# Kernel tuning notes

Measured on AMD Instinct MI355X. Metric: run time of the kernel, lower is better.

## Reference

```python
import jax, jax.numpy as jnp
import numpy as np

N_ENT = 50000
N_REL2 = 100   # num_relations * 2
N_BASES = 16
DIM = 64
N_EDGES = 100000


def _rgcn_conv(x, edge_index, edge_type, edge_norm, basis, att, root, bias):
    # x: [N, D]; basis: [B, D, D]; att: [R, B]; root: [D, D]; bias: [D]
    src = edge_index[0]
    dst = edge_index[1]
    num_nodes = x.shape[0]
    # Per-edge relation weight is w[edge_type] with w = att @ basis (reshaped).
    # By linearity we contract x_j with each basis first, then mix with the
    # per-edge attention coefficients -- same math, avoids the [E, D, D] gather.
    coeff = att[edge_type]                          # [E, B]
    xb = jnp.einsum('ei,bio->ebo', x[src], basis)   # [E, B, D]
    msg = jnp.einsum('eb,ebo->eo', coeff, xb)       # [E, D]
    msg = msg * edge_norm[:, None]
    # scatter-mean aggregation at target nodes
    s = jax.ops.segment_sum(msg, dst, num_segments=num_nodes)
    cnt = jax.ops.segment_sum(jnp.ones((msg.shape[0],), msg.dtype), dst,
                              num_segments=num_nodes)
    agg = s / jnp.maximum(cnt, 1.0)[:, None]
    # root transform + bias
    return agg + x @ root + bias


def setup_inputs() -> dict:
    key = jax.random.key(0)
    ks = jax.random.split(key, 12)
    E = N_EDGES
    inp = {
        'entity': jnp.arange(N_ENT, dtype=jnp.int64) if jax.config.jax_enable_x64 else jnp.arange(N_ENT, dtype=jnp.int32),
        'edge_index': jax.random.randint(ks[0], (2, E), 0, N_ENT),
        'edge_type': jax.random.randint(ks[1], (E,), 0, N_REL2),
        'edge_norm': jax.random.uniform(ks[2], (E,), dtype=jnp.float32),
        'emb': jax.random.normal(ks[3], (N_ENT, DIM), dtype=jnp.float32) * 0.1,
        'basis1': jax.random.normal(ks[4], (N_BASES, DIM, DIM), dtype=jnp.float32) * 0.05,
        'att1': jax.random.normal(ks[5], (N_REL2, N_BASES), dtype=jnp.float32) * 0.1,
        'root1': jax.random.normal(ks[6], (DIM, DIM), dtype=jnp.float32) * 0.05,
        'bias1': jnp.zeros((DIM,), dtype=jnp.float32),
        'basis2': jax.random.normal(ks[7], (N_BASES, DIM, DIM), dtype=jnp.float32) * 0.05,
        'att2': jax.random.normal(ks[8], (N_REL2, N_BASES), dtype=jnp.float32) * 0.1,
        'root2': jax.random.normal(ks[9], (DIM, DIM), dtype=jnp.float32) * 0.05,
        'bias2': jnp.zeros((DIM,), dtype=jnp.float32),
    }
    return inp


def reference(entity, edge_index, edge_type, edge_norm, emb,
              basis1, att1, root1, bias1, basis2, att2, root2, bias2):
    x = emb[entity]                                  # embedding lookup [N, D]
    x = _rgcn_conv(x, edge_index, edge_type, edge_norm, basis1, att1, root1, bias1)
    x = _rgcn_conv(x, edge_index, edge_type, edge_norm, basis2, att2, root2, bias2)
    return x
```

## Files before the change

kernel.cpp:

```cpp
#include <hip/hip_runtime.h>

#define NN 50000
#define NR 100
#define NB 16
#define D  64
#define NE 100000

#define HB  196
#define EPB 512

#define CHUNK 128
#define GROUPS 2
#define EGRID 1024

#define NPB 128
#define NGRID ((NN + NPB - 1) / NPB)

typedef float f32x4  __attribute__((ext_vector_type(4)));
typedef short bf16x8 __attribute__((ext_vector_type(8)));

__device__ __forceinline__ short f2bf(float f) {
    unsigned u = __float_as_uint(f);
    return (short)((u + 0x7FFFu + ((u >> 16) & 1u)) >> 16);
}

__device__ __forceinline__ bf16x8 pack8(f32x4 a, f32x4 b) {
    bf16x8 t;
    t[0] = f2bf(a.x); t[1] = f2bf(a.y); t[2] = f2bf(a.z); t[3] = f2bf(a.w);
    t[4] = f2bf(b.x); t[5] = f2bf(b.y); t[6] = f2bf(b.z); t[7] = f2bf(b.w);
    return t;
}

__global__ __launch_bounds__(256) void compute_wt(
    const float* __restrict__ att1, const float* __restrict__ basis1,
    const float* __restrict__ root1,
    const float* __restrict__ att2, const float* __restrict__ basis2,
    const float* __restrict__ root2,
    float* __restrict__ Wt1, float* __restrict__ Wt2,
    float* __restrict__ rT1, float* __restrict__ rT2)
{
    __shared__ float t[64 * 65];
    int b = blockIdx.x;
    if (b < 2 * NR) {
        int layer = b >= NR;
        int r = layer ? b - NR : b;
        const float* att   = layer ? att2 : att1;
        const float* basis = layer ? basis2 : basis1;
        float*       Wt    = layer ? Wt2 : Wt1;
        float a[NB];
#pragma unroll
        for (int bb = 0; bb < NB; ++bb) a[bb] = att[r * NB + bb];
#pragma unroll
        for (int i = 0; i < 16; ++i) {
            int idx = i * 256 + threadIdx.x;
            float acc = 0.f;
#pragma unroll
            for (int bb = 0; bb < NB; ++bb) acc += a[bb] * basis[bb * 4096 + idx];
            t[(idx >> 6) * 65 + (idx & 63)] = acc;
        }
        __syncthreads();
#pragma unroll
        for (int i = 0; i < 16; ++i) {
            int j = i * 256 + threadIdx.x;
            Wt[(size_t)r * 4096 + j] = t[(j & 63) * 65 + (j >> 6)];
        }
    } else {
        const float* root = (b == 2 * NR) ? root1 : root2;
        float*       rT   = (b == 2 * NR) ? rT1 : rT2;
#pragma unroll
        for (int i = 0; i < 16; ++i) {
            int idx = i * 256 + threadIdx.x;
            t[(idx >> 6) * 65 + (idx & 63)] = root[idx];
        }
        __syncthreads();
#pragma unroll
        for (int i = 0; i < 16; ++i) {
            int j = i * 256 + threadIdx.x;
            rT[j] = t[(j & 63) * 65 + (j >> 6)];
        }
    }
}

__global__ __launch_bounds__(256) void gather_zero(
    const int* __restrict__ entity, const f32x4* __restrict__ emb4,
    f32x4* __restrict__ x04, f32x4* __restrict__ s4, f32x4* __restrict__ cnt4)
{
    int idx = blockIdx.x * 256 + threadIdx.x;
    if (idx >= NN * 16) return;
    int n = idx >> 4;
    int q = idx & 15;
    f32x4 z = {0.f, 0.f, 0.f, 0.f};
    x04[idx] = emb4[(size_t)entity[n] * 16 + q];
    s4[idx] = z;
    if (idx < NN / 4) cnt4[idx] = z;
}

__global__ __launch_bounds__(256) void hist_edges(
    const int* __restrict__ et, const int* __restrict__ dst,
    int* __restrict__ blockHist, float* __restrict__ cnt)
{
    __shared__ int lh[NR];
    for (int i = threadIdx.x; i < NR; i += 256) lh[i] = 0;
    __syncthreads();
#pragma unroll
    for (int i = 0; i < EPB / 256; ++i) {
        int e = blockIdx.x * EPB + i * 256 + threadIdx.x;
        if (e < NE) {
            atomicAdd(&lh[et[e]], 1);
            atomicAdd(&cnt[dst[e]], 1.0f);
        }
    }
    __syncthreads();
    for (int i = threadIdx.x; i < NR; i += 256)
        blockHist[blockIdx.x * NR + i] = lh[i];
}

__global__ __launch_bounds__(256) void colscan(
    const int* __restrict__ blockHist, int* __restrict__ blockPrefix,
    int* __restrict__ relTot)
{
    __shared__ int sc[256];
    int r = blockIdx.x;
    int t = threadIdx.x;
    int v = (t < HB) ? blockHist[t * NR + r] : 0;
    sc[t] = v;
    __syncthreads();
#pragma unroll
    for (int off = 1; off < 256; off <<= 1) {
        int a = (t >= off) ? sc[t - off] : 0;
        __syncthreads();
        sc[t] += a;
        __syncthreads();
    }
    if (t < HB) blockPrefix[t * NR + r] = sc[t] - v;
    if (t == 0) relTot[r] = sc[255];
}

__global__ __launch_bounds__(256) void scanK(
    const int* __restrict__ relTot, int* __restrict__ offs,
    int* __restrict__ nbG, int* __restrict__ tabR, int* __restrict__ tabS)
{
    __shared__ int totL[NR];
    __shared__ int offL[NR + 1];
    __shared__ int cnbL[NR + 1];
    int t = threadIdx.x;
    if (t < NR) totL[t] = relTot[t];
    __syncthreads();
    if (t == 0) {
        int off = 0, cb = 0;
        for (int r = 0; r < NR; ++r) {
            offL[r] = off; cnbL[r] = cb;
            off += totL[r];
            cb  += (totL[r] + CHUNK - 1) / CHUNK;
        }
        offL[NR] = off; cnbL[NR] = cb;
    }
    __syncthreads();
    if (t <= NR) offs[t] = offL[t];
    if (t == 0) nbG[0] = cnbL[NR];
    int nb = cnbL[NR];
    for (int e = t; e < nb; e += 256) {
        int lo = 0, hi = NR;
        while (hi - lo > 1) { int mid = (lo + hi) >> 1; if (cnbL[mid] <= e) lo = mid; else hi = mid; }
        tabR[e] = lo;
        tabS[e] = offL[lo] + (e - cnbL[lo]) * CHUNK;
    }
}

__global__ __launch_bounds__(256) void scatter_sorted(
    const int* __restrict__ src, const int* __restrict__ dst,
    const int* __restrict__ et, const float* __restrict__ en,
    const int* __restrict__ offs, const int* __restrict__ blockPrefix,
    int* __restrict__ srcS, int* __restrict__ dstS, float* __restrict__ normS)
{
    __shared__ int lcur[NR];
    for (int i = threadIdx.x; i < NR; i += 256)
        lcur[i] = offs[i] + blockPrefix[blockIdx.x * NR + i];
    __syncthreads();
#pragma unroll
    for (int i = 0; i < EPB / 256; ++i) {
        int e = blockIdx.x * EPB + i * 256 + threadIdx.x;
        if (e < NE) {
            int r = et[e];
            int p = atomicAdd(&lcur[r], 1);
            srcS[p] = src[e]; dstS[p] = dst[e]; normS[p] = en[e];
        }
    }
}

__global__ __launch_bounds__(256, 4) void edge_mfma(
    const int* __restrict__ srcS, const int* __restrict__ dstS,
    const float* __restrict__ normS, const int* __restrict__ offs,
    const int* __restrict__ tabR, const int* __restrict__ tabS,
    const int* __restrict__ nbG, const float* __restrict__ x,
    const float* __restrict__ Wt, float* __restrict__ s)
{
    __shared__ float LW[64 * 68];
    int b = blockIdx.x;
    if (b >= nbG[0]) return;
    int r  = tabR[b];
    int cs = tabS[b];
    int tid = threadIdx.x;

    {
        const f32x4* __restrict__ Wg = (const f32x4*)(Wt + (size_t)r * 4096);
#pragma unroll
        for (int i = 0; i < 4; ++i) {
            int v = tid + i * 256;
            int d = v >> 4, k4 = v & 15;
            *(f32x4*)(LW + d * 68 + k4 * 4) = Wg[v];
        }
    }
    __syncthreads();

    int lane = tid & 63, wid = tid >> 6;
    int c15 = lane & 15, kg = lane >> 4;

    bf16x8 B[4][2];
#pragma unroll
    for (int nt = 0; nt < 4; ++nt)
#pragma unroll
        for (int ks = 0; ks < 2; ++ks) {
            const f32x4* p = (const f32x4*)(LW + (nt * 16 + c15) * 68 + ks * 32 + kg * 8);
            B[nt][ks] = pack8(p[0], p[1]);
        }

    int segE = offs[r + 1];
    int bend = cs + CHUNK < segE ? cs + CHUNK : segE;

#pragma unroll 1
    for (int g = 0; g < GROUPS; ++g) {
        int gs = cs + wid * (GROUPS * 16) + g * 16;
        if (gs >= bend) break;
        int ge = gs + 16 < bend ? gs + 16 : bend;

        int e  = gs + c15;
        int ec = e < ge ? e : ge - 1;
        float nrm = (e < ge) ? normS[ec] : 0.f;
        int   sn  = srcS[ec];

        const f32x4* xr  = (const f32x4*)(x + (size_t)sn * 64 + kg * 8);
        const f32x4* xr2 = (const f32x4*)(x + (size_t)sn * 64 + 32 + kg * 8);
        bf16x8 A0 = pack8(xr[0]  * nrm, xr[1]  * nrm);
        bf16x8 A1 = pack8(xr2[0] * nrm, xr2[1] * nrm);

        f32x4 z = {0.f, 0.f, 0.f, 0.f};
        f32x4 acc[4] = {z, z, z, z};
#pragma unroll
        for (int nt = 0; nt < 4; ++nt) {
            acc[nt] = __builtin_amdgcn_mfma_f32_16x16x32_bf16(A0, B[nt][0], acc[nt], 0, 0, 0);
            acc[nt] = __builtin_amdgcn_mfma_f32_16x16x32_bf16(A1, B[nt][1], acc[nt], 0, 0, 0);
        }

        int dn[4];
#pragma unroll
        for (int j = 0; j < 4; ++j) {
            int er = gs + kg * 4 + j;
            dn[j] = (er < ge) ? dstS[er] : -1;
        }
#pragma unroll
        for (int nt = 0; nt < 4; ++nt)
#pragma unroll
            for (int j = 0; j < 4; ++j)
                if (dn[j] >= 0)
                    atomicAdd(&s[(size_t)dn[j] * 64 + nt * 16 + c15], acc[nt][j]);
    }
}

__global__ __launch_bounds__(256, 4) void node_mfma(
    const float* __restrict__ x, float* __restrict__ s,
    const float* __restrict__ cnt, const float* __restrict__ rT,
    const float* __restrict__ bias, float* __restrict__ out, int zero_s)
{
    __shared__ float LW[64 * 68];
    int tid = threadIdx.x;
    {
        const f32x4* __restrict__ Rg = (const f32x4*)rT;
#pragma unroll
        for (int i = 0; i < 4; ++i) {
            int v = tid + i * 256;
            int d = v >> 4, k4 = v & 15;
            *(f32x4*)(LW + d * 68 + k4 * 4) = Rg[v];
        }
    }
    __syncthreads();

    int lane = tid & 63, wid = tid >> 6;
    int c15 = lane & 15, kg = lane >> 4;

    bf16x8 B[4][2];
#pragma unroll
    for (int nt = 0; nt < 4; ++nt)
#pragma unroll
        for (int ks = 0; ks < 2; ++ks) {
            const f32x4* p = (const f32x4*)(LW + (nt * 16 + c15) * 68 + ks * 32 + kg * 8);
            B[nt][ks] = pack8(p[0], p[1]);
        }
    float bv[4];
#pragma unroll
    for (int nt = 0; nt < 4; ++nt) bv[nt] = bias[nt * 16 + c15];

#pragma unroll 1
    for (int g = 0; g < GROUPS; ++g) {
        int gs = blockIdx.x * NPB + wid * (GROUPS * 16) + g * 16;
        if (gs >= NN) break;
        int ge = gs + 16 < NN ? gs + 16 : NN;

        int n  = gs + c15;
        int nc = n < ge ? n : ge - 1;
        const f32x4* xr  = (const f32x4*)(x + (size_t)nc * 64 + kg * 8);
        const f32x4* xr2 = (const f32x4*)(x + (size_t)nc * 64 + 32 + kg * 8);
        bf16x8 A0 = pack8(xr[0], xr[1]);
        bf16x8 A1 = pack8(xr2[0], xr2[1]);

        f32x4 z = {0.f, 0.f, 0.f, 0.f};
        f32x4 acc[4] = {z, z, z, z};
#pragma unroll
        for (int nt = 0; nt < 4; ++nt) {
            acc[nt] = __builtin_amdgcn_mfma_f32_16x16x32_bf16(A0, B[nt][0], acc[nt], 0, 0, 0);
            acc[nt] = __builtin_amdgcn_mfma_f32_16x16x32_bf16(A1, B[nt][1], acc[nt], 0, 0, 0);
        }

        float cv[4];
#pragma unroll
        for (int j = 0; j < 4; ++j) {
            int nr = gs + kg * 4 + j;
            cv[j] = (nr < ge) ? cnt[nr] : 1.f;
        }
#pragma unroll
        for (int nt = 0; nt < 4; ++nt)
#pragma unroll
            for (int j = 0; j < 4; ++j) {
                int nr = gs + kg * 4 + j;
                if (nr < ge) {
                    size_t off = (size_t)nr * 64 + nt * 16 + c15;
                    float c = cv[j] > 1.f ? cv[j] : 1.f;
                    out[off] = s[off] / c + acc[nt][j] + bv[nt];
                    if (zero_s) s[off] = 0.f;
                }
            }
    }
}

extern "C" void kernel_launch(void* const* d_in, const int* in_sizes, int n_in,
                              void* d_out, int out_size, void* d_ws, size_t ws_size,
                              hipStream_t stream) {
    const int*   entity    = (const int*)d_in[0];
    const int*   edge_index= (const int*)d_in[1];
    const int*   edge_type = (const int*)d_in[2];
    const float* edge_norm = (const float*)d_in[3];
    const float* emb       = (const float*)d_in[4];
    const float* basis1    = (const float*)d_in[5];
    const float* att1      = (const float*)d_in[6];
    const float* root1     = (const float*)d_in[7];
    const float* bias1     = (const float*)d_in[8];
    const float* basis2    = (const float*)d_in[9];
    const float* att2      = (const float*)d_in[10];
    const float* root2     = (const float*)d_in[11];
    const float* bias2     = (const float*)d_in[12];

    const int* src = edge_index;
    const int* dst = edge_index + NE;

    float* ws    = (float*)d_ws;
    float* Wt1   = ws;
    float* Wt2   = Wt1 + (size_t)NR * 4096;
    float* rT1   = Wt2 + (size_t)NR * 4096;
    float* rT2   = rT1 + 4096;
    float* x0    = rT2 + 4096;
    float* s     = x0  + (size_t)NN * D;
    float* cnt   = s   + (size_t)NN * D;
    float* normS = cnt + NN;
    int*   offs        = (int*)(normS + NE);
    int*   relTot      = offs + NR + 3;
    int*   nbG         = relTot + NR;
    int*   blockHist   = nbG + 3;
    int*   blockPrefix = blockHist + HB * NR;
    int*   tabR        = blockPrefix + HB * NR;
    int*   tabS        = tabR + EGRID;
    int*   srcS        = tabS + EGRID;
    int*   dstS        = srcS + NE;

    float* out = (float*)d_out;

    compute_wt<<<2 * NR + 2, 256, 0, stream>>>(att1, basis1, root1,
                                               att2, basis2, root2,
                                               Wt1, Wt2, rT1, rT2);
    gather_zero<<<(NN * 16 + 255) / 256, 256, 0, stream>>>(
        entity, (const f32x4*)emb, (f32x4*)x0, (f32x4*)s, (f32x4*)cnt);
    hist_edges<<<HB, 256, 0, stream>>>(edge_type, dst, blockHist, cnt);
    colscan<<<NR, 256, 0, stream>>>(blockHist, blockPrefix, relTot);
    scanK<<<1, 256, 0, stream>>>(relTot, offs, nbG, tabR, tabS);
    scatter_sorted<<<HB, 256, 0, stream>>>(src, dst, edge_type, edge_norm,
                                           offs, blockPrefix, srcS, dstS, normS);

    edge_mfma<<<EGRID, 256, 0, stream>>>(srcS, dstS, normS, offs,
                                         tabR, tabS, nbG, x0, Wt1, s);
    node_mfma<<<NGRID, 256, 0, stream>>>(x0, s, cnt, rT1, bias1, out, 1);

    edge_mfma<<<EGRID, 256, 0, stream>>>(srcS, dstS, normS, offs,
                                         tabR, tabS, nbG, out, Wt2, s);
    node_mfma<<<NGRID, 256, 0, stream>>>(out, s, cnt, rT2, bias2, out, 0);
}
```

Baseline: 127.6 us.

## Replace atomic scatter-add with CSR gather aggregation by destination node

Edge kernels now write per-edge messages to a dense msg buffer instead of doing float atomics into s. A per-destination CSR index (degree histogram, node prefix scan, dstIdx permutation) is built during preprocessing, and node_mfma gathers and averages incoming messages per node before adding the root transform. Zeroing of s and cnt is dropped and the embedding gather is merged into the weight-prep kernel. The aim is to remove atomic contention on the aggregation. In exchange it writes and re-reads a 100000x64 message buffer and uses a serial per-node gather loop with uneven degrees.

```diff
diff --git a/kernel.cpp b/kernel.cpp
--- a/kernel.cpp
+++ b/kernel.cpp
@@ -8,6 +8,8 @@
 
 #define HB  196
 #define EPB 512
+#define ZB  196
+#define GB  ((NN * 16 + 255) / 256)
 
 #define CHUNK 128
 #define GROUPS 2
@@ -31,13 +33,15 @@
     return t;
 }
 
-__global__ __launch_bounds__(256) void compute_wt(
+__global__ __launch_bounds__(256) void prep_all(
     const float* __restrict__ att1, const float* __restrict__ basis1,
     const float* __restrict__ root1,
     const float* __restrict__ att2, const float* __restrict__ basis2,
     const float* __restrict__ root2,
+    const int* __restrict__ entity, const f32x4* __restrict__ emb4,
     float* __restrict__ Wt1, float* __restrict__ Wt2,
-    float* __restrict__ rT1, float* __restrict__ rT2)
+    float* __restrict__ rT1, float* __restrict__ rT2,
+    f32x4* __restrict__ x04, int* __restrict__ deg, int* __restrict__ nodeCur)
 {
     __shared__ float t[64 * 65];
     int b = blockIdx.x;
@@ -64,7 +68,7 @@
             int j = i * 256 + threadIdx.x;
             Wt[(size_t)r * 4096 + j] = t[(j & 63) * 65 + (j >> 6)];
         }
-    } else {
+    } else if (b < 2 * NR + 2) {
         const float* root = (b == 2 * NR) ? root1 : root2;
         float*       rT   = (b == 2 * NR) ? rT1 : rT2;
 #pragma unroll
@@ -78,26 +82,22 @@
             int j = i * 256 + threadIdx.x;
             rT[j] = t[(j & 63) * 65 + (j >> 6)];
         }
-    }
-}
-
-__global__ __launch_bounds__(256) void gather_zero(
-    const int* __restrict__ entity, const f32x4* __restrict__ emb4,
-    f32x4* __restrict__ x04, f32x4* __restrict__ s4, f32x4* __restrict__ cnt4)
-{
-    int idx = blockIdx.x * 256 + threadIdx.x;
-    if (idx >= NN * 16) return;
-    int n = idx >> 4;
-    int q = idx & 15;
-    f32x4 z = {0.f, 0.f, 0.f, 0.f};
-    x04[idx] = emb4[(size_t)entity[n] * 16 + q];
-    s4[idx] = z;
-    if (idx < NN / 4) cnt4[idx] = z;
+    } else if (b < 2 * NR + 2 + ZB) {
+        int i = (b - (2 * NR + 2)) * 256 + threadIdx.x;
+        deg[i] = 0; nodeCur[i] = 0;
+    } else {
+        int idx = (b - (2 * NR + 2 + ZB)) * 256 + threadIdx.x;
+        if (idx < NN * 16) {
+            int n = idx >> 4;
+            int q = idx & 15;
+            x04[idx] = emb4[(size_t)entity[n] * 16 + q];
+        }
+    }
 }
 
 __global__ __launch_bounds__(256) void hist_edges(
     const int* __restrict__ et, const int* __restrict__ dst,
-    int* __restrict__ blockHist, float* __restrict__ cnt)
+    int* __restrict__ blockHist, int* __restrict__ deg)
 {
     __shared__ int lh[NR];
     for (int i = threadIdx.x; i < NR; i += 256) lh[i] = 0;
@@ -107,7 +107,7 @@
         int e = blockIdx.x * EPB + i * 256 + threadIdx.x;
         if (e < NE) {
             atomicAdd(&lh[et[e]], 1);
-            atomicAdd(&cnt[dst[e]], 1.0f);
+            atomicAdd(&deg[dst[e]], 1);
         }
     }
     __syncthreads();
@@ -115,36 +115,59 @@
         blockHist[blockIdx.x * NR + i] = lh[i];
 }
 
-__global__ __launch_bounds__(256) void colscan(
+__global__ __launch_bounds__(256) void scans(
     const int* __restrict__ blockHist, int* __restrict__ blockPrefix,
-    int* __restrict__ relTot)
+    int* __restrict__ relTot, const int* __restrict__ deg,
+    int* __restrict__ nodePre, int* __restrict__ blockSumN)
 {
     __shared__ int sc[256];
-    int r = blockIdx.x;
     int t = threadIdx.x;
-    int v = (t < HB) ? blockHist[t * NR + r] : 0;
-    sc[t] = v;
-    __syncthreads();
-#pragma unroll
-    for (int off = 1; off < 256; off <<= 1) {
-        int a = (t >= off) ? sc[t - off] : 0;
-        __syncthreads();
-        sc[t] += a;
-        __syncthreads();
-    }
-    if (t < HB) blockPrefix[t * NR + r] = sc[t] - v;
-    if (t == 0) relTot[r] = sc[255];
+    if (blockIdx.x < NR) {
+        int r = blockIdx.x;
+        int v = (t < HB) ? blockHist[t * NR + r] : 0;
+        sc[t] = v;
+        __syncthreads();
+#pragma unroll
+        for (int off = 1; off < 256; off <<= 1) {
+            int a = (t >= off) ? sc[t - off] : 0;
+            __syncthreads();
+            sc[t] += a;
+            __syncthreads();
+        }
+        if (t < HB) blockPrefix[t * NR + r] = sc[t] - v;
+        if (t == 0) relTot[r] = sc[255];
+    } else {
+        int b = blockIdx.x - NR;
+        int n = b * 256 + t;
+        int v = deg[n];
+        sc[t] = v;
+        __syncthreads();
+#pragma unroll
+        for (int off = 1; off < 256; off <<= 1) {
+            int a = (t >= off) ? sc[t - off] : 0;
+            __syncthreads();
+            sc[t] += a;
+            __syncthreads();
+        }
+        nodePre[n] = sc[t] - v;
+        if (t == 255) blockSumN[b] = sc[255];
+    }
 }
 
 __global__ __launch_bounds__(256) void scanK(
-    const int* __restrict__ relTot, int* __restrict__ offs,
-    int* __restrict__ nbG, int* __restrict__ tabR, int* __restrict__ tabS)
+    const int* __restrict__ relTot, const int* __restrict__ blockSumN,
+    int* __restrict__ offs, int* __restrict__ nbG,
+    int* __restrict__ tabR, int* __restrict__ tabS,
+    int* __restrict__ nodeBlockBase)
 {
     __shared__ int totL[NR];
     __shared__ int offL[NR + 1];
     __shared__ int cnbL[NR + 1];
+    __shared__ int sc2[256];
     int t = threadIdx.x;
     if (t < NR) totL[t] = relTot[t];
+    int v2 = (t < ZB) ? blockSumN[t] : 0;
+    sc2[t] = v2;
     __syncthreads();
     if (t == 0) {
         int off = 0, cb = 0;
@@ -156,6 +179,15 @@
         offL[NR] = off; cnbL[NR] = cb;
     }
     __syncthreads();
+#pragma unroll
+    for (int off = 1; off < 256; off <<= 1) {
+        int a = (t >= off) ? sc2[t - off] : 0;
+        __syncthreads();
+        sc2[t] += a;
+        __syncthreads();
+    }
+    if (t < ZB) nodeBlockBase[t] = sc2[t] - v2;
+    if (t == 0) nodeBlockBase[ZB] = sc2[255];
     if (t <= NR) offs[t] = offL[t];
     if (t == 0) nbG[0] = cnbL[NR];
     int nb = cnbL[NR];
@@ -167,11 +199,13 @@
     }
 }
 
-__global__ __launch_bounds__(256) void scatter_sorted(
+__global__ __launch_bounds__(256) void scatter2(
     const int* __restrict__ src, const int* __restrict__ dst,
     const int* __restrict__ et, const float* __restrict__ en,
     const int* __restrict__ offs, const int* __restrict__ blockPrefix,
-    int* __restrict__ srcS, int* __restrict__ dstS, float* __restrict__ normS)
+    const int* __restrict__ nodePre, const int* __restrict__ nodeBlockBase,
+    int* __restrict__ nodeCur, int* __restrict__ srcS,
+    float* __restrict__ normS, int* __restrict__ dstIdx)
 {
     __shared__ int lcur[NR];
     for (int i = threadIdx.x; i < NR; i += 256)
@@ -183,17 +217,20 @@
         if (e < NE) {
             int r = et[e];
             int p = atomicAdd(&lcur[r], 1);
-            srcS[p] = src[e]; dstS[p] = dst[e]; normS[p] = en[e];
+            srcS[p] = src[e]; normS[p] = en[e];
+            int n = dst[e];
+            int q = nodeBlockBase[n >> 8] + nodePre[n] + atomicAdd(&nodeCur[n], 1);
+            dstIdx[q] = p;
         }
     }
 }
 
 __global__ __launch_bounds__(256, 4) void edge_mfma(
-    const int* __restrict__ srcS, const int* __restrict__ dstS,
-    const float* __restrict__ normS, const int* __restrict__ offs,
-    const int* __restrict__ tabR, const int* __restrict__ tabS,
-    const int* __restrict__ nbG, const float* __restrict__ x,
-    const float* __restrict__ Wt, float* __restrict__ s)
+    const int* __restrict__ srcS, const float* __restrict__ normS,
+    const int* __restrict__ offs, const int* __restrict__ tabR,
+    const int* __restrict__ tabS, const int* __restrict__ nbG,
+    const float* __restrict__ x, const float* __restrict__ Wt,
+    float* __restrict__ msg)
 {
     __shared__ float LW[64 * 68];
     int b = blockIdx.x;
@@ -251,28 +288,25 @@
             acc[nt] = __builtin_amdgcn_mfma_f32_16x16x32_bf16(A0, B[nt][0], acc[nt], 0, 0, 0);
             acc[nt] = __builtin_amdgcn_mfma_f32_16x16x32_bf16(A1, B[nt][1], acc[nt], 0, 0, 0);
         }
-
-        int dn[4];
-#pragma unroll
-        for (int j = 0; j < 4; ++j) {
-            int er = gs + kg * 4 + j;
-            dn[j] = (er < ge) ? dstS[er] : -1;
-        }
 #pragma unroll
         for (int nt = 0; nt < 4; ++nt)
 #pragma unroll
-            for (int j = 0; j < 4; ++j)
-                if (dn[j] >= 0)
-                    atomicAdd(&s[(size_t)dn[j] * 64 + nt * 16 + c15], acc[nt][j]);
+            for (int j = 0; j < 4; ++j) {
+                int er = gs + kg * 4 + j;
+                if (er < ge)
+                    msg[(size_t)er * 64 + nt * 16 + c15] = acc[nt][j];
+            }
     }
 }
 
 __global__ __launch_bounds__(256, 4) void node_mfma(
-    const float* __restrict__ x, float* __restrict__ s,
-    const float* __restrict__ cnt, const float* __restrict__ rT,
-    const float* __restrict__ bias, float* __restrict__ out, int zero_s)
+    const float* __restrict__ x, const float* __restrict__ msg,
+    const int* __restrict__ dstIdx, const int* __restrict__ nodePre,
+    const int* __restrict__ nodeBlockBase, const float* __restrict__ rT,
+    const float* __restrict__ bias, float* __restrict__ out)
 {
     __shared__ float LW[64 * 68];
+    __shared__ float aggL[4][32][68];
     int tid = threadIdx.x;
     {
         const f32x4* __restrict__ Rg = (const f32x4*)rT;
@@ -300,9 +334,28 @@
 #pragma unroll
     for (int nt = 0; nt < 4; ++nt) bv[nt] = bias[nt * 16 + c15];
 
+    int wbase = blockIdx.x * NPB + wid * 32;
+    if (wbase >= NN) return;
+
 #pragma unroll 1
-    for (int g = 0; g < GROUPS; ++g) {
-        int gs = blockIdx.x * NPB + wid * (GROUPS * 16) + g * 16;
+    for (int ln = 0; ln < 32; ++ln) {
+        int n = wbase + ln;
+        if (n >= NN) break;
+        int blk  = n >> 8;
+        int base = nodeBlockBase[blk];
+        int lo = base + nodePre[n];
+        int hi = ((n & 255) == 255) ? nodeBlockBase[blk + 1] : base + nodePre[n + 1];
+        float acc = 0.f;
+        for (int q = lo; q < hi; ++q)
+            acc += msg[(size_t)dstIdx[q] * 64 + lane];
+        float c = (float)(hi - lo);
+        c = c > 1.f ? c : 1.f;
+        aggL[wid][ln][lane] = acc / c;
+    }
+
+#pragma unroll 1
+    for (int g = 0; g < 2; ++g) {
+        int gs = wbase + g * 16;
         if (gs >= NN) break;
         int ge = gs + 16 < NN ? gs + 16 : NN;
 
@@ -320,24 +373,14 @@
             acc[nt] = __builtin_amdgcn_mfma_f32_16x16x32_bf16(A0, B[nt][0], acc[nt], 0, 0, 0);
             acc[nt] = __builtin_amdgcn_mfma_f32_16x16x32_bf16(A1, B[nt][1], acc[nt], 0, 0, 0);
         }
-
-        float cv[4];
-#pragma unroll
-        for (int j = 0; j < 4; ++j) {
-            int nr = gs + kg * 4 + j;
-            cv[j] = (nr < ge) ? cnt[nr] : 1.f;
-        }
 #pragma unroll
         for (int nt = 0; nt < 4; ++nt)
 #pragma unroll
             for (int j = 0; j < 4; ++j) {
                 int nr = gs + kg * 4 + j;
-                if (nr < ge) {
-                    size_t off = (size_t)nr * 64 + nt * 16 + c15;
-                    float c = cv[j] > 1.f ? cv[j] : 1.f;
-                    out[off] = s[off] / c + acc[nt][j] + bv[nt];
-                    if (zero_s) s[off] = 0.f;
-                }
+                if (nr < ge)
+                    out[(size_t)nr * 64 + nt * 16 + c15] =
+                        aggL[wid][g * 16 + kg * 4 + j][nt * 16 + c15] + acc[nt][j] + bv[nt];
             }
     }
 }
@@ -368,9 +411,8 @@
     float* rT1   = Wt2 + (size_t)NR * 4096;
     float* rT2   = rT1 + 4096;
     float* x0    = rT2 + 4096;
-    float* s     = x0  + (size_t)NN * D;
-    float* cnt   = s   + (size_t)NN * D;
-    float* normS = cnt + NN;
+    float* msg   = x0  + (size_t)NN * D;
+    float* normS = msg + (size_t)NE * D;
     int*   offs        = (int*)(normS + NE);
     int*   relTot      = offs + NR + 3;
     int*   nbG         = relTot + NR;
@@ -379,26 +421,34 @@
     int*   tabR        = blockPrefix + HB * NR;
     int*   tabS        = tabR + EGRID;
     int*   srcS        = tabS + EGRID;
-    int*   dstS        = srcS + NE;
+    int*   deg         = srcS + NE;
+    int*   nodePre     = deg + ZB * 256;
+    int*   nodeCur     = nodePre + ZB * 256;
+    int*   blockSumN   = nodeCur + ZB * 256;
+    int*   nodeBB      = blockSumN + ZB + 4;
+    int*   dstIdx      = nodeBB + ZB + 5;
 
     float* out = (float*)d_out;
 
-    compute_wt<<<2 * NR + 2, 256, 0, stream>>>(att1, basis1, root1,
-                                               att2, basis2, root2,
-                                               Wt1, Wt2, rT1, rT2);
-    gather_zero<<<(NN * 16 + 255) / 256, 256, 0, stream>>>(
-        entity, (const f32x4*)emb, (f32x4*)x0, (f32x4*)s, (f32x4*)cnt);
-    hist_edges<<<HB, 256, 0, stream>>>(edge_type, dst, blockHist, cnt);
-    colscan<<<NR, 256, 0, stream>>>(blockHist, blockPrefix, relTot);
-    scanK<<<1, 256, 0, stream>>>(relTot, offs, nbG, tabR, tabS);
-    scatter_sorted<<<HB, 256, 0, stream>>>(src, dst, edge_type, edge_norm,
-                                           offs, blockPrefix, srcS, dstS, normS);
-
-    edge_mfma<<<EGRID, 256, 0, stream>>>(srcS, dstS, normS, offs,
-                                         tabR, tabS, nbG, x0, Wt1, s);
-    node_mfma<<<NGRID, 256, 0, stream>>>(x0, s, cnt, rT1, bias1, out, 1);
-
-    edge_mfma<<<EGRID, 256, 0, stream>>>(srcS, dstS, normS, offs,
-                                         tabR, tabS, nbG, out, Wt2, s);
-    node_mfma<<<NGRID, 256, 0, stream>>>(out, s, cnt, rT2, bias2, out, 0);
-}
+    prep_all<<<2 * NR + 2 + ZB + GB, 256, 0, stream>>>(
+        att1, basis1, root1, att2, basis2, root2,
+        entity, (const f32x4*)emb, Wt1, Wt2, rT1, rT2,
+        (f32x4*)x0, deg, nodeCur);
+    hist_edges<<<HB, 256, 0, stream>>>(edge_type, dst, blockHist, deg);
+    scans<<<NR + ZB, 256, 0, stream>>>(blockHist, blockPrefix, relTot,
+                                       deg, nodePre, blockSumN);
+    scanK<<<1, 256, 0, stream>>>(relTot, blockSumN, offs, nbG, tabR, tabS, nodeBB);
+    scatter2<<<HB, 256, 0, stream>>>(src, dst, edge_type, edge_norm,
+                                     offs, blockPrefix, nodePre, nodeBB,
+                                     nodeCur, srcS, normS, dstIdx);
+
+    edge_mfma<<<EGRID, 256, 0, stream>>>(srcS, normS, offs, tabR, tabS, nbG,
+                                         x0, Wt1, msg);
+    node_mfma<<<NGRID, 256, 0, stream>>>(x0, msg, dstIdx, nodePre, nodeBB,
+                                         rT1, bias1, out);
+
+    edge_mfma<<<EGRID, 256, 0, stream>>>(srcS, normS, offs, tabR, tabS, nbG,
+                                         out, Wt2, msg);
+    node_mfma<<<NGRID, 256, 0, stream>>>(out, msg, dstIdx, nodePre, nodeBB,
+                                         rT2, bias2, out);
+}
```

Result: slower. 176.0 us (+37.9%).
